# Kernel tuning notes

Hardware: AMD Instinct MI355X
Metric: run time of the kernel (lower is better)

The kernel has to match this reference:

```python
import jax, jax.numpy as jnp
import numpy as np

DIM = 256
NUM_HEADS = 4
HEAD_DIM = DIM // NUM_HEADS
LN_EPS = 1e-5


def setup_inputs() -> dict:
    key = jax.random.key(0)
    ks = jax.random.split(key, 5)
    B, C, H, W = 4, DIM, 64, 64
    x = jax.random.normal(ks[0], (B, C, H, W), dtype=jnp.float32)
    ln_g = jnp.ones((DIM,), dtype=jnp.float32)
    ln_b = jnp.zeros((DIM,), dtype=jnp.float32)
    # torch Linear init scale ~ 1/sqrt(fan_in)
    w_qkv = jax.random.normal(ks[1], (DIM, 3 * DIM), dtype=jnp.float32) / np.sqrt(DIM)
    w_proj = jax.random.normal(ks[2], (DIM, DIM), dtype=jnp.float32) / np.sqrt(DIM)
    b_proj = jax.random.normal(ks[3], (DIM,), dtype=jnp.float32) * 0.01
    return {"x": x, "ln_g": ln_g, "ln_b": ln_b, "w_qkv": w_qkv,
            "w_proj": w_proj, "b_proj": b_proj}


def _attention_block(x, ln_g, ln_b, w_qkv, w_proj, b_proj):
    B, C, H, W = x.shape
    N = H * W
    h, d = NUM_HEADS, HEAD_DIM
    # b c h w -> b n c
    t = x.reshape(B, C, N).transpose(0, 2, 1)
    # LayerNorm over channel dim
    mu = jnp.mean(t, axis=-1, keepdims=True)
    var = jnp.mean(jnp.square(t - mu), axis=-1, keepdims=True)
    t = (t - mu) * jax.lax.rsqrt(var + LN_EPS) * ln_g + ln_b
    # qkv projection (no bias); layout of last dim is (three, heads, d)
    qkv = t @ w_qkv  # [B, N, 3*C]
    qkv = qkv.reshape(B, N, 3, h, d)
    q = qkv[:, :, 0].transpose(0, 2, 1, 3)  # [B, h, N, d]
    k = qkv[:, :, 1].transpose(0, 2, 1, 3)
    v = qkv[:, :, 2].transpose(0, 2, 1, 3)
    # scaled dot-product attention (original chunks over queries; same math)
    scale = 1.0 / jnp.sqrt(jnp.asarray(d, dtype=q.dtype))
    dots = jnp.einsum('bhnd,bhmd->bhnm', q, k) * scale
    attn = jax.nn.softmax(dots, axis=-1)
    o = jnp.einsum('bhnm,bhmd->bhnd', attn, v)  # [B, h, N, d]
    # b h n d -> b n (h d)
    o = o.transpose(0, 2, 1, 3).reshape(B, N, C)
    o = o @ w_proj.T + b_proj  # torch Linear convention not needed; keep explicit
    # b n c -> b c h w
    return o.transpose(0, 2, 1).reshape(B, C, H, W)


def reference(x, ln_g, ln_b, w_qkv, w_proj, b_proj):
    return _attention_block(x, ln_g, ln_b, w_qkv, w_proj, b_proj)
```

## Files before the change

kernel.cpp:

```cpp
#include <hip/hip_runtime.h>
#include <math.h>

#define NB 4
#define NC 256
#define NHEADS 4
#define DH 64
#define NT 4096
#define QSCALE (0.125f * 1.44269504088896f)

typedef __bf16  bf16x8 __attribute__((ext_vector_type(8)));
typedef __bf16  bf16x4 __attribute__((ext_vector_type(4)));
typedef float   f32x4  __attribute__((ext_vector_type(4)));
typedef short   s16x8  __attribute__((ext_vector_type(8)));

static __device__ __forceinline__ unsigned short f2bf(float f) {
    unsigned u = __float_as_uint(f);
    u = (u + 0x7fffu + ((u >> 16) & 1u)) >> 16;
    return (unsigned short)u;
}

static __device__ __forceinline__ float fast_exp2(float x) {
    return __builtin_amdgcn_exp2f(x);
}

static __device__ __forceinline__ void gload16(const unsigned short* g, unsigned short* l) {
    __builtin_amdgcn_global_load_lds((const __attribute__((address_space(1))) void*)g,
                                     (__attribute__((address_space(3))) void*)l, 16, 0, 0);
}

static __device__ __forceinline__ void stage_64x256(
    unsigned short* __restrict__ lds, const unsigned short* __restrict__ g, int tid)
{
    #pragma unroll
    for (int chunk = 0; chunk < 8; ++chunk) {
        const int row = chunk * 8 + (tid >> 5);
        const int col = (tid & 31) * 8;
        *(s16x8*)&lds[row * 264 + col] = *(const s16x8*)&g[row * 256 + col];
    }
}

__global__ __launch_bounds__(256) void k_prep(
    const float* __restrict__ wqkv, const float* __restrict__ wproj,
    unsigned short* __restrict__ wqkv_t, unsigned short* __restrict__ wproj_bf)
{
    const int id = blockIdx.x;
    const int tid = threadIdx.x;
    if (id < 48) {
        __shared__ float T[64][65];
        const int jt = id % 12, ct = id / 12;
        #pragma unroll
        for (int p = 0; p < 16; ++p) {
            const int idx = tid + (p << 8);
            const int r = idx >> 6, cl = idx & 63;
            T[r][cl] = wqkv[(size_t)(ct * 64 + r) * 768 + jt * 64 + cl];
        }
        __syncthreads();
        #pragma unroll
        for (int p = 0; p < 16; ++p) {
            const int idx = tid + (p << 8);
            const int r = idx >> 6, cl = idx & 63;
            wqkv_t[(size_t)(jt * 64 + r) * 256 + ct * 64 + cl] = f2bf(T[cl][r]);
        }
    } else {
        const int base = (id - 48) * 2048 + tid * 8;
        s16x8 v;
        #pragma unroll
        for (int j = 0; j < 8; ++j) v[j] = (short)f2bf(wproj[base + j]);
        *(s16x8*)&wproj_bf[base] = v;
    }
}

__global__ __launch_bounds__(256) void k_ln_qkv(
    const float* __restrict__ x,
    const float* __restrict__ ln_g,
    const float* __restrict__ ln_b,
    const unsigned short* __restrict__ wqkv_t,
    unsigned short* __restrict__ q_bf,
    unsigned short* __restrict__ k_bf,
    unsigned short* __restrict__ v_bf)
{
    __shared__ unsigned short An[64 * 264];
    __shared__ unsigned short Wt[64 * 264];
    __shared__ float red1[4][64], red2[4][64];
    __shared__ float mu_s[64], rs_s[64];

    const int b     = blockIdx.x >> 6;
    const int n0    = (blockIdx.x & 63) << 6;
    const int three = blockIdx.y;
    const int tid   = threadIdx.x;
    const int li    = tid & 63;
    const int grp   = tid >> 6;
    const int w     = grp;
    const int lane  = li;
    const int q4    = lane >> 4;
    const int c     = lane & 15;

    const float* xb = x + ((size_t)b * NC) * NT + n0 + li;

    float xr[64];
    #pragma unroll
    for (int chunk = 0; chunk < 8; ++chunk)
        #pragma unroll
        for (int j = 0; j < 8; ++j)
            xr[chunk * 8 + j] = xb[(size_t)(chunk * 32 + grp * 8 + j) * NT];

    float s1 = 0.f, s2 = 0.f;
    #pragma unroll
    for (int i = 0; i < 64; ++i) { s1 += xr[i]; s2 += xr[i] * xr[i]; }
    red1[grp][li] = s1; red2[grp][li] = s2;
    __syncthreads();
    if (tid < 64) {
        const float t1 = red1[0][tid] + red1[1][tid] + red1[2][tid] + red1[3][tid];
        const float t2 = red2[0][tid] + red2[1][tid] + red2[2][tid] + red2[3][tid];
        const float mu  = t1 * (1.0f / NC);
        const float var = t2 * (1.0f / NC) - mu * mu;
        mu_s[tid] = mu;
        rs_s[tid] = rsqrtf(var + 1e-5f);
    }
    __syncthreads();
    const float mu = mu_s[li];
    const float rs = rs_s[li];

    #pragma unroll
    for (int chunk = 0; chunk < 8; ++chunk) {
        s16x8 pk;
        #pragma unroll
        for (int j = 0; j < 8; ++j) {
            const int ch = chunk * 32 + grp * 8 + j;
            const float vv = (xr[chunk * 8 + j] - mu) * rs * ln_g[ch] + ln_b[ch];
            pk[j] = (short)f2bf(vv);
        }
        *(s16x8*)&An[li * 264 + chunk * 32 + grp * 8] = pk;
    }
    __syncthreads();

    bf16x8 aT[8];
    if (three < 2) {
        #pragma unroll
        for (int kt = 0; kt < 8; ++kt)
            aT[kt] = *(const bf16x8*)&An[(16 * w + c) * 264 + kt * 32 + q4 * 8];
    }

    for (int jt = 0; jt < 4; ++jt) {
        __syncthreads();
        stage_64x256(Wt, wqkv_t + (size_t)(three * 256 + jt * 64) * 256, tid);
        __syncthreads();

        f32x4 acc[4];
        #pragma unroll
        for (int nt = 0; nt < 4; ++nt)
            #pragma unroll
            for (int r = 0; r < 4; ++r) acc[nt][r] = 0.f;

        const int bh = b * NHEADS + jt;
        if (three < 2) {
            #pragma unroll
            for (int nt = 0; nt < 4; ++nt)
                #pragma unroll
                for (int kt = 0; kt < 8; ++kt) {
                    const bf16x8 bb = *(const bf16x8*)&Wt[(16 * nt + c) * 264 + kt * 32 + q4 * 8];
                    acc[nt] = __builtin_amdgcn_mfma_f32_16x16x32_bf16(aT[kt], bb, acc[nt], 0, 0, 0);
                }
            unsigned short* dst = (three == 0 ? q_bf : k_bf) + ((size_t)bh * NT + n0) * DH;
            const float sc = (three == 0) ? QSCALE : 1.0f;
            #pragma unroll
            for (int nt = 0; nt < 4; ++nt)
                #pragma unroll
                for (int r = 0; r < 4; ++r)
                    dst[(size_t)(16 * w + 4 * q4 + r) * DH + 16 * nt + c] = f2bf(acc[nt][r] * sc);
        } else {
            bf16x8 aW[8];
            #pragma unroll
            for (int kt = 0; kt < 8; ++kt)
                aW[kt] = *(const bf16x8*)&Wt[(16 * w + c) * 264 + kt * 32 + q4 * 8];
            #pragma unroll
            for (int nt = 0; nt < 4; ++nt)
                #pragma unroll
                for (int kt = 0; kt < 8; ++kt) {
                    const bf16x8 bb = *(const bf16x8*)&An[(16 * nt + c) * 264 + kt * 32 + q4 * 8];
                    acc[nt] = __builtin_amdgcn_mfma_f32_16x16x32_bf16(aW[kt], bb, acc[nt], 0, 0, 0);
                }
            unsigned short* dst = v_bf + (size_t)bh * DH * NT;
            #pragma unroll
            for (int nt = 0; nt < 4; ++nt)
                #pragma unroll
                for (int r = 0; r < 4; ++r)
                    dst[(size_t)(16 * w + 4 * q4 + r) * NT + n0 + 16 * nt + c] = f2bf(acc[nt][r]);
        }
    }
}

__global__ __launch_bounds__(256, 2) void k_attn(
    const unsigned short* __restrict__ qg,
    const unsigned short* __restrict__ kg,
    const unsigned short* __restrict__ vg,
    float* __restrict__ o_part,
    float* __restrict__ l_part)
{
    __shared__ unsigned short Ks[2 * 4096];
    __shared__ unsigned short Vt[2 * 4096];
    __shared__ __bf16 Ps[256 * 72];

    const int bh   = blockIdx.x >> 5;
    const int rest = blockIdx.x & 31;
    const int qt   = rest >> 1;
    const int kh   = rest & 1;
    const int n0   = qt << 8;
    const int tid  = threadIdx.x;
    const int w    = tid >> 6;
    const int lane = tid & 63;
    const int q4   = lane >> 4;
    const int c    = lane & 15;

    const unsigned short* kb = kg + ((size_t)bh * NT + (kh << 11)) * DH;
    const unsigned short* vb = vg + (size_t)bh * DH * NT + (kh << 11);

    bf16x8 aq[4][2];
    {
        const unsigned short* qp = qg + ((size_t)bh * NT + n0) * DH;
        #pragma unroll
        for (int g = 0; g < 4; ++g) {
            const unsigned short* qrow = qp + (size_t)(64 * w + 16 * g + c) * DH;
            aq[g][0] = *(const bf16x8*)(qrow + q4 * 8);
            aq[g][1] = *(const bf16x8*)(qrow + 32 + q4 * 8);
        }
    }

    const int rr = lane >> 3;
    const int kc = (lane & 7) ^ rr;
    const int koffK = rr * DH + kc * 8;

    const int sw0 = ((q4    ) ^ (c & 7)) * 8;
    const int sw1 = ((q4 + 4) ^ (c & 7)) * 8;

    #define ISSUE_TILE(it_, bi_)                                               \
        {                                                                      \
            const unsigned short* ktp = kb + (size_t)(it_) * 64 * DH;          \
            const unsigned short* vtp = vb + (size_t)(it_) * 64;               \
            _Pragma("unroll")                                                  \
            for (int t = 0; t < 2; ++t) {                                      \
                const int grp_ = w * 2 + t;                                    \
                gload16(ktp + grp_ * 512 + koffK,                              \
                        &Ks[(bi_) * 4096 + grp_ * 512 + lane * 8]);            \
                gload16(vtp + (size_t)(grp_ * 8 + rr) * NT + kc * 8,           \
                        &Vt[(bi_) * 4096 + grp_ * 512 + lane * 8]);            \
            }                                                                  \
        }

    ISSUE_TILE(0, 0)

    f32x4 oac[4][4];
    #pragma unroll
    for (int g = 0; g < 4; ++g)
        #pragma unroll
        for (int dt = 0; dt < 4; ++dt)
            #pragma unroll
            for (int r = 0; r < 4; ++r) oac[g][dt][r] = 0.f;
    float lsum[4][4] = {};

    for (int it = 0; it < 32; ++it) {
        const int cur = it & 1;
        asm volatile("s_waitcnt vmcnt(0)\n\ts_barrier" ::: "memory");
        if (it < 31) ISSUE_TILE(it + 1, cur ^ 1)

        const unsigned short* Kb = &Ks[cur * 4096];
        const unsigned short* Vb = &Vt[cur * 4096];

        #pragma unroll
        for (int nt = 0; nt < 4; ++nt) {
            const bf16x8 kf0 = *(const bf16x8*)&Kb[(16 * nt + c) * 64 + sw0];
            const bf16x8 kf1 = *(const bf16x8*)&Kb[(16 * nt + c) * 64 + sw1];
            #pragma unroll
            for (int g = 0; g < 4; ++g) {
                f32x4 acc;
                #pragma unroll
                for (int r = 0; r < 4; ++r) acc[r] = 0.f;
                acc = __builtin_amdgcn_mfma_f32_16x16x32_bf16(kf0, aq[g][0], acc, 0, 0, 0);
                acc = __builtin_amdgcn_mfma_f32_16x16x32_bf16(kf1, aq[g][1], acc, 0, 0, 0);
                bf16x4 pk;
                #pragma unroll
                for (int r = 0; r < 4; ++r) {
                    const float e = fast_exp2(acc[r]);
                    lsum[g][nt] += e;
                    pk[r] = (__bf16)e;
                }
                *(bf16x4*)&Ps[(64 * w + 16 * g + c) * 72 + 16 * nt + 4 * q4] = pk;
            }
        }

        bf16x8 pa[4][2];
        #pragma unroll
        for (int g = 0; g < 4; ++g) {
            const __bf16* prow = &Ps[(64 * w + 16 * g + c) * 72];
            pa[g][0] = *(const bf16x8*)(prow + q4 * 8);
            pa[g][1] = *(const bf16x8*)(prow + 32 + q4 * 8);
        }
        #pragma unroll
        for (int dt = 0; dt < 4; ++dt) {
            const bf16x8 v0 = *(const bf16x8*)&Vb[(16 * dt + c) * 64 + sw0];
            const bf16x8 v1 = *(const bf16x8*)&Vb[(16 * dt + c) * 64 + sw1];
            #pragma unroll
            for (int g = 0; g < 4; ++g) {
                oac[g][dt] = __builtin_amdgcn_mfma_f32_16x16x32_bf16(pa[g][0], v0, oac[g][dt], 0, 0, 0);
                oac[g][dt] = __builtin_amdgcn_mfma_f32_16x16x32_bf16(pa[g][1], v1, oac[g][dt], 0, 0, 0);
            }
        }
    }
    #undef ISSUE_TILE

    float* op = o_part + (((size_t)kh * 16 + bh) * NT + n0 + 64 * w) * DH;
    #pragma unroll
    for (int g = 0; g < 4; ++g)
        #pragma unroll
        for (int dt = 0; dt < 4; ++dt)
            #pragma unroll
            for (int r = 0; r < 4; ++r)
                op[(size_t)(16 * g + 4 * q4 + r) * DH + 16 * dt + c] = oac[g][dt][r];

    float* lp = l_part + ((size_t)kh * 16 + bh) * NT + n0 + 64 * w;
    #pragma unroll
    for (int g = 0; g < 4; ++g) {
        float t = (lsum[g][0] + lsum[g][1]) + (lsum[g][2] + lsum[g][3]);
        t += __shfl_xor(t, 16);
        t += __shfl_xor(t, 32);
        if (q4 == 0) lp[16 * g + c] = t;
    }
}

__global__ __launch_bounds__(256) void k_proj(
    const float* __restrict__ o_part,
    const float* __restrict__ l_part,
    const unsigned short* __restrict__ wproj_bf,
    const float* __restrict__ b_proj,
    float* __restrict__ out)
{
    __shared__ unsigned short Os[64 * 264];
    __shared__ unsigned short Ws[64 * 264];

    const int b   = blockIdx.x >> 6;
    const int n0  = (blockIdx.x & 63) << 6;
    const int yh  = blockIdx.y;
    const int tid = threadIdx.x;
    const int w   = tid >> 6;
    const int lane = tid & 63;
    const int q4  = lane >> 4;
    const int c   = lane & 15;

    const size_t OPS = (size_t)16 * NT * DH;
    const size_t LPS = (size_t)16 * NT;

    #pragma unroll
    for (int chunk = 0; chunk < 8; ++chunk) {
        const int row = chunk * 8 + (tid >> 5);
        const int col = (tid & 31) * 8;
        const int hd  = col >> 6;
        const int c64 = col & 63;
        const size_t tok = (size_t)(b * NHEADS + hd) * NT + n0 + row;
        const float rv = 1.0f / (l_part[tok] + l_part[LPS + tok]);
        const float* p0 = o_part + tok * DH + c64;
        const float* p1 = p0 + OPS;
        const f32x4 a0 = *(const f32x4*)p0;
        const f32x4 a1 = *(const f32x4*)(p0 + 4);
        const f32x4 b0 = *(const f32x4*)p1;
        const f32x4 b1 = *(const f32x4*)(p1 + 4);
        s16x8 pk;
        #pragma unroll
        for (int j = 0; j < 4; ++j) {
            pk[j]     = (short)f2bf((a0[j] + b0[j]) * rv);
            pk[4 + j] = (short)f2bf((a1[j] + b1[j]) * rv);
        }
        *(s16x8*)&Os[row * 264 + col] = pk;
    }

    for (int ct = 0; ct < 2; ++ct) {
        const int cg0 = (yh * 2 + ct) * 64;
        if (ct) __syncthreads();
        stage_64x256(Ws, wproj_bf + (size_t)cg0 * NC, tid);
        __syncthreads();

        bf16x8 a[8];
        #pragma unroll
        for (int kt = 0; kt < 8; ++kt)
            a[kt] = *(const bf16x8*)&Ws[(16 * w + c) * 264 + kt * 32 + q4 * 8];

        f32x4 acc[4];
        #pragma unroll
        for (int nt = 0; nt < 4; ++nt)
            #pragma unroll
            for (int r = 0; r < 4; ++r) acc[nt][r] = 0.f;

        #pragma unroll
        for (int nt = 0; nt < 4; ++nt)
            #pragma unroll
            for (int kt = 0; kt < 8; ++kt) {
                const bf16x8 bb = *(const bf16x8*)&Os[(16 * nt + c) * 264 + kt * 32 + q4 * 8];
                acc[nt] = __builtin_amdgcn_mfma_f32_16x16x32_bf16(a[kt], bb, acc[nt], 0, 0, 0);
            }

        #pragma unroll
        for (int nt = 0; nt < 4; ++nt)
            #pragma unroll
            for (int r = 0; r < 4; ++r) {
                const int cg = cg0 + 16 * w + 4 * q4 + r;
                out[((size_t)b * NC + cg) * NT + n0 + 16 * nt + c] = acc[nt][r] + b_proj[cg];
            }
    }
}

extern "C" void kernel_launch(void* const* d_in, const int* in_sizes, int n_in,
                              void* d_out, int out_size, void* d_ws, size_t ws_size,
                              hipStream_t stream)
{
    const float* x      = (const float*)d_in[0];
    const float* ln_g   = (const float*)d_in[1];
    const float* ln_b   = (const float*)d_in[2];
    const float* w_qkv  = (const float*)d_in[3];
    const float* w_proj = (const float*)d_in[4];
    const float* b_proj = (const float*)d_in[5];
    float* out = (float*)d_out;

    const size_t TEN = (size_t)NB * NHEADS * NT * DH;

    float* ws32 = (float*)d_ws;
    float* o_part = ws32;
    float* l_part = ws32 + 8388608;
    unsigned short* ws16 = (unsigned short*)(l_part + 131072);
    unsigned short* q_bf    = ws16;
    unsigned short* k_bf    = ws16 + TEN;
    unsigned short* v_bf    = ws16 + 2 * TEN;
    unsigned short* wqkv_t  = ws16 + 3 * TEN;
    unsigned short* wproj_b = wqkv_t + 768 * 256;

    k_prep<<<80, 256, 0, stream>>>(w_qkv, w_proj, wqkv_t, wproj_b);
    k_ln_qkv<<<dim3(NB * 64, 3), 256, 0, stream>>>(x, ln_g, ln_b, wqkv_t, q_bf, k_bf, v_bf);
    k_attn<<<16 * 32, 256, 0, stream>>>(q_bf, k_bf, v_bf, o_part, l_part);
    k_proj<<<dim3(NB * 64, 2), 256, 0, stream>>>(o_part, l_part, wproj_b, b_proj, out);
}
```

Baseline: 190.3 us.

## Rework attention to 32x32 MFMA with in-register P via permlane swap

The attention kernel switches from 16x16x32 to 32x32x16 bf16 MFMA, with each wave owning 32 query rows instead of 64. The exponentiated scores are packed to bf16 and redistributed in registers with v_permlane32_swap, so the LDS round-trip for P is gone. Removing the P scratch frees LDS, which allows 4 blocks per CU and twice as many blocks. Block indices are also swizzled across XCDs. Each block still loads every K/V tile, so K/V traffic per query roughly doubles, and the new lane mapping has to match the MFMA operand layout exactly.

```diff
diff --git a/kernel.cpp b/kernel.cpp
--- a/kernel.cpp
+++ b/kernel.cpp
@@ -11,7 +11,9 @@
 typedef __bf16  bf16x8 __attribute__((ext_vector_type(8)));
 typedef __bf16  bf16x4 __attribute__((ext_vector_type(4)));
 typedef float   f32x4  __attribute__((ext_vector_type(4)));
+typedef float   f32x16 __attribute__((ext_vector_type(16)));
 typedef short   s16x8  __attribute__((ext_vector_type(8)));
+typedef unsigned int u32x4 __attribute__((ext_vector_type(4)));
 
 static __device__ __forceinline__ unsigned short f2bf(float f) {
     unsigned u = __float_as_uint(f);
@@ -21,6 +23,20 @@
 
 static __device__ __forceinline__ float fast_exp2(float x) {
     return __builtin_amdgcn_exp2f(x);
+}
+
+static __device__ __forceinline__ unsigned cvtpk(float lo, float hi) {
+    unsigned r;
+    asm("v_cvt_pk_bf16_f32 %0, %1, %2" : "=v"(r) : "v"(lo), "v"(hi));
+    return r;
+}
+
+static __device__ __forceinline__ void plswap(unsigned &a, unsigned &b) {
+    asm("v_permlane32_swap_b32 %0, %1" : "+v"(a), "+v"(b));
+}
+
+static __device__ __forceinline__ bf16x8 as_bf16x8(u32x4 v) {
+    return __builtin_bit_cast(bf16x8, v);
 }
 
 static __device__ __forceinline__ void gload16(const unsigned short* g, unsigned short* l) {
@@ -190,7 +206,7 @@
     }
 }
 
-__global__ __launch_bounds__(256, 2) void k_attn(
+__global__ __launch_bounds__(256, 4) void k_attn(
     const unsigned short* __restrict__ qg,
     const unsigned short* __restrict__ kg,
     const unsigned short* __restrict__ vg,
@@ -199,39 +215,33 @@
 {
     __shared__ unsigned short Ks[2 * 4096];
     __shared__ unsigned short Vt[2 * 4096];
-    __shared__ __bf16 Ps[256 * 72];
-
-    const int bh   = blockIdx.x >> 5;
-    const int rest = blockIdx.x & 31;
-    const int qt   = rest >> 1;
-    const int kh   = rest & 1;
-    const int n0   = qt << 8;
+
+    const int bx   = ((blockIdx.x & 7) << 7) | (blockIdx.x >> 3);
+    const int bh   = bx >> 6;
+    const int qt   = (bx >> 1) & 31;
+    const int kh   = bx & 1;
+    const int n0   = qt << 7;
     const int tid  = threadIdx.x;
     const int w    = tid >> 6;
     const int lane = tid & 63;
-    const int q4   = lane >> 4;
-    const int c    = lane & 15;
+    const int c5   = lane & 31;
+    const int hi   = lane >> 5;
+    const int qb   = n0 + (w << 5);
 
     const unsigned short* kb = kg + ((size_t)bh * NT + (kh << 11)) * DH;
     const unsigned short* vb = vg + (size_t)bh * DH * NT + (kh << 11);
 
-    bf16x8 aq[4][2];
+    bf16x8 aq[4];
     {
-        const unsigned short* qp = qg + ((size_t)bh * NT + n0) * DH;
-        #pragma unroll
-        for (int g = 0; g < 4; ++g) {
-            const unsigned short* qrow = qp + (size_t)(64 * w + 16 * g + c) * DH;
-            aq[g][0] = *(const bf16x8*)(qrow + q4 * 8);
-            aq[g][1] = *(const bf16x8*)(qrow + 32 + q4 * 8);
-        }
+        const unsigned short* qrow = qg + ((size_t)bh * NT + qb + c5) * DH + hi * 8;
+        #pragma unroll
+        for (int ks = 0; ks < 4; ++ks)
+            aq[ks] = *(const bf16x8*)(qrow + ks * 16);
     }
 
     const int rr = lane >> 3;
     const int kc = (lane & 7) ^ rr;
     const int koffK = rr * DH + kc * 8;
-
-    const int sw0 = ((q4    ) ^ (c & 7)) * 8;
-    const int sw1 = ((q4 + 4) ^ (c & 7)) * 8;
 
     #define ISSUE_TILE(it_, bi_)                                               \
         {                                                                      \
@@ -249,14 +259,14 @@
 
     ISSUE_TILE(0, 0)
 
-    f32x4 oac[4][4];
-    #pragma unroll
-    for (int g = 0; g < 4; ++g)
-        #pragma unroll
-        for (int dt = 0; dt < 4; ++dt)
-            #pragma unroll
-            for (int r = 0; r < 4; ++r) oac[g][dt][r] = 0.f;
-    float lsum[4][4] = {};
+    f32x16 oac[2];
+    #pragma unroll
+    for (int dt = 0; dt < 2; ++dt)
+        #pragma unroll
+        for (int r = 0; r < 16; ++r) oac[dt][r] = 0.f;
+    float lsum = 0.f;
+
+    const int swz = (c5 & 7);
 
     for (int it = 0; it < 32; ++it) {
         const int cur = it & 1;
@@ -267,64 +277,66 @@
         const unsigned short* Vb = &Vt[cur * 4096];
 
         #pragma unroll
-        for (int nt = 0; nt < 4; ++nt) {
-            const bf16x8 kf0 = *(const bf16x8*)&Kb[(16 * nt + c) * 64 + sw0];
-            const bf16x8 kf1 = *(const bf16x8*)&Kb[(16 * nt + c) * 64 + sw1];
-            #pragma unroll
-            for (int g = 0; g < 4; ++g) {
-                f32x4 acc;
-                #pragma unroll
-                for (int r = 0; r < 4; ++r) acc[r] = 0.f;
-                acc = __builtin_amdgcn_mfma_f32_16x16x32_bf16(kf0, aq[g][0], acc, 0, 0, 0);
-                acc = __builtin_amdgcn_mfma_f32_16x16x32_bf16(kf1, aq[g][1], acc, 0, 0, 0);
-                bf16x4 pk;
-                #pragma unroll
-                for (int r = 0; r < 4; ++r) {
-                    const float e = fast_exp2(acc[r]);
-                    lsum[g][nt] += e;
-                    pk[r] = (__bf16)e;
-                }
-                *(bf16x4*)&Ps[(64 * w + 16 * g + c) * 72 + 16 * nt + 4 * q4] = pk;
+        for (int sb = 0; sb < 2; ++sb) {
+            f32x16 sacc;
+            #pragma unroll
+            for (int r = 0; r < 16; ++r) sacc[r] = 0.f;
+            #pragma unroll
+            for (int ks = 0; ks < 4; ++ks) {
+                const bf16x8 kf = *(const bf16x8*)
+                    &Kb[(sb * 32 + c5) * 64 + (((2 * ks + hi) ^ swz) << 3)];
+                sacc = __builtin_amdgcn_mfma_f32_32x32x16_bf16(kf, aq[ks], sacc, 0, 0, 0);
             }
-        }
-
-        bf16x8 pa[4][2];
-        #pragma unroll
-        for (int g = 0; g < 4; ++g) {
-            const __bf16* prow = &Ps[(64 * w + 16 * g + c) * 72];
-            pa[g][0] = *(const bf16x8*)(prow + q4 * 8);
-            pa[g][1] = *(const bf16x8*)(prow + 32 + q4 * 8);
-        }
-        #pragma unroll
-        for (int dt = 0; dt < 4; ++dt) {
-            const bf16x8 v0 = *(const bf16x8*)&Vb[(16 * dt + c) * 64 + sw0];
-            const bf16x8 v1 = *(const bf16x8*)&Vb[(16 * dt + c) * 64 + sw1];
-            #pragma unroll
-            for (int g = 0; g < 4; ++g) {
-                oac[g][dt] = __builtin_amdgcn_mfma_f32_16x16x32_bf16(pa[g][0], v0, oac[g][dt], 0, 0, 0);
-                oac[g][dt] = __builtin_amdgcn_mfma_f32_16x16x32_bf16(pa[g][1], v1, oac[g][dt], 0, 0, 0);
+
+            #pragma unroll
+            for (int r = 0; r < 16; ++r) {
+                sacc[r] = fast_exp2(sacc[r]);
+                lsum += sacc[r];
             }
+
+            unsigned X0 = cvtpk(sacc[0],  sacc[1]);
+            unsigned X1 = cvtpk(sacc[4],  sacc[5]);
+            plswap(X0, X1);
+            unsigned X2 = cvtpk(sacc[2],  sacc[3]);
+            unsigned X3 = cvtpk(sacc[6],  sacc[7]);
+            plswap(X2, X3);
+            const u32x4 paA = (u32x4){X0, X2, X1, X3};
+
+            unsigned Y0 = cvtpk(sacc[8],  sacc[9]);
+            unsigned Y1 = cvtpk(sacc[12], sacc[13]);
+            plswap(Y0, Y1);
+            unsigned Y2 = cvtpk(sacc[10], sacc[11]);
+            unsigned Y3 = cvtpk(sacc[14], sacc[15]);
+            plswap(Y2, Y3);
+            const u32x4 paB = (u32x4){Y0, Y2, Y1, Y3};
+
+            #pragma unroll
+            for (int dt = 0; dt < 2; ++dt) {
+                const bf16x8 vA = *(const bf16x8*)
+                    &Vb[(dt * 32 + c5) * 64 + (((4 * sb + hi) ^ swz) << 3)];
+                oac[dt] = __builtin_amdgcn_mfma_f32_32x32x16_bf16(
+                    as_bf16x8(paA), vA, oac[dt], 0, 0, 0);
+                const bf16x8 vB = *(const bf16x8*)
+                    &Vb[(dt * 32 + c5) * 64 + (((4 * sb + 2 + hi) ^ swz) << 3)];
+                oac[dt] = __builtin_amdgcn_mfma_f32_32x32x16_bf16(
+                    as_bf16x8(paB), vB, oac[dt], 0, 0, 0);
+            }
         }
     }
     #undef ISSUE_TILE
 
-    float* op = o_part + (((size_t)kh * 16 + bh) * NT + n0 + 64 * w) * DH;
-    #pragma unroll
-    for (int g = 0; g < 4; ++g)
-        #pragma unroll
-        for (int dt = 0; dt < 4; ++dt)
-            #pragma unroll
-            for (int r = 0; r < 4; ++r)
-                op[(size_t)(16 * g + 4 * q4 + r) * DH + 16 * dt + c] = oac[g][dt][r];
-
-    float* lp = l_part + ((size_t)kh * 16 + bh) * NT + n0 + 64 * w;
-    #pragma unroll
-    for (int g = 0; g < 4; ++g) {
-        float t = (lsum[g][0] + lsum[g][1]) + (lsum[g][2] + lsum[g][3]);
-        t += __shfl_xor(t, 16);
-        t += __shfl_xor(t, 32);
-        if (q4 == 0) lp[16 * g + c] = t;
-    }
+    float* op = o_part + (((size_t)kh * 16 + bh) * NT + qb) * DH;
+    #pragma unroll
+    for (int dt = 0; dt < 2; ++dt)
+        #pragma unroll
+        for (int r = 0; r < 16; ++r) {
+            const int qrow = (r & 3) + 8 * (r >> 2) + 4 * hi;
+            op[(size_t)qrow * DH + 32 * dt + c5] = oac[dt][r];
+        }
+
+    float t = lsum + __shfl_xor(lsum, 32);
+    if (lane < 32)
+        l_part[((size_t)kh * 16 + bh) * NT + qb + c5] = t;
 }
 
 __global__ __launch_bounds__(256) void k_proj(
@@ -433,6 +445,6 @@
 
     k_prep<<<80, 256, 0, stream>>>(w_qkv, w_proj, wqkv_t, wproj_b);
     k_ln_qkv<<<dim3(NB * 64, 3), 256, 0, stream>>>(x, ln_g, ln_b, wqkv_t, q_bf, k_bf, v_bf);
-    k_attn<<<16 * 32, 256, 0, stream>>>(q_bf, k_bf, v_bf, o_part, l_part);
+    k_attn<<<16 * 64, 256, 0, stream>>>(q_bf, k_bf, v_bf, o_part, l_part);
     k_proj<<<dim3(NB * 64, 2), 256, 0, stream>>>(o_part, l_part, wproj_b, b_proj, out);
 }
```

After: 194.1 us. +2.0%, slower.
